# Optimization experiments

Hardware: AMD Instinct MI355X
Metric: run time of the kernel (lower is better)

Reference implementation:

```python
import jax, jax.numpy as jnp
import numpy as np

N_NODES = 50000
N_EDGES = 800000
D_FEAT = 128
UNITS = 128


def setup_inputs() -> dict:
    key = jax.random.key(0)
    k1, k2, k3, k4 = jax.random.split(key, 4)
    x = jax.random.normal(k1, (N_NODES, D_FEAT), dtype=jnp.float32)
    source = jax.random.randint(k2, (N_EDGES,), 0, N_NODES, dtype=jnp.int32)
    target = jax.random.randint(k3, (N_EDGES,), 0, N_NODES, dtype=jnp.int32)
    W = jax.random.normal(k4, (D_FEAT, UNITS), dtype=jnp.float32) * (1.0 / np.sqrt(D_FEAT))
    b = jnp.zeros((UNITS,), dtype=jnp.float32)
    return {"x": x, "source": source, "target": target, "W": W, "b": b}


def _degree(idx, n_nodes):
    # in/out degree = segment-sum of unit edge weights; clamp to >= 1 (no self loops)
    deg = jnp.zeros((n_nodes,), dtype=jnp.float32).at[idx].add(1.0)
    return jnp.maximum(deg, 1.0)


def reference(x, source, target, W, b):
    n = x.shape[0]
    # degree_normalization == "in_out": sender scale from out-degree, receiver from in-degree
    sender_scale = jax.lax.rsqrt(_degree(source, n))[:, None]      # [N, 1]
    receiver_scale = jax.lax.rsqrt(_degree(target, n))[:, None]    # [N, 1]
    normalized = sender_scale * x                                  # [N, D]
    source_bcast = normalized[source]                              # [E, D] gather
    pooled = jax.ops.segment_sum(source_bcast, target, num_segments=n)  # [N, D] scatter-add
    pooled = receiver_scale * pooled
    # Dense(units, activation='relu', use_bias=True)
    return jax.nn.relu(pooled @ W + b)
```

## Files before the change

kernel.cpp:

```cpp
#include <hip/hip_runtime.h>
#include <hip/hip_bf16.h>

#define N_FEAT 128
#define EPT 8
#define CHUNK 2048
#define BSHIFT 8
#define MAXRANGE 256
#define CAP 8192

typedef short bf16x8 __attribute__((ext_vector_type(8)));
typedef float f32x4  __attribute__((ext_vector_type(4)));

__device__ __forceinline__ unsigned short f2bf_rtne(float f) {
    unsigned u = __float_as_uint(f);
    u += 0x7fffu + ((u >> 16) & 1u);
    return (unsigned short)(u >> 16);
}
__device__ __forceinline__ float bf2f(unsigned short h) {
    return __uint_as_float((unsigned)h << 16);
}

__global__ __launch_bounds__(256) void scatter_kernel(const int* __restrict__ source,
                                                      const int* __restrict__ target,
                                                      int* __restrict__ curT,
                                                      int* __restrict__ curS,
                                                      unsigned int* __restrict__ pairsT,
                                                      unsigned char* __restrict__ srcB,
                                                      int E, int NB) {
    __shared__ unsigned int   lds_pairs[CHUNK];
    __shared__ unsigned short lds_sp[CHUNK];
    __shared__ int ct[MAXRANGE], cs[MAXRANGE];
    __shared__ int st[MAXRANGE], ss[MAXRANGE];
    __shared__ int gt[MAXRANGE], gs[MAXRANGE];
    int tid = threadIdx.x, b = blockIdx.x;
    int base = b * CHUNK;
    int cnt = E - base; if (cnt > CHUNK) cnt = CHUNK;

    ct[tid] = 0; cs[tid] = 0;
    __syncthreads();
    #pragma unroll
    for (int j = 0; j < EPT; ++j) {
        int e = base + j * 256 + tid;
        if (e < E) {
            atomicAdd(&ct[target[e] >> BSHIFT], 1);
            atomicAdd(&cs[source[e] >> BSHIFT], 1);
        }
    }
    __syncthreads();
    int vt = ct[tid], vs = cs[tid];
    st[tid] = vt; ss[tid] = vs;
    __syncthreads();
    #pragma unroll
    for (int off = 1; off < 256; off <<= 1) {
        int t1 = (tid >= off) ? st[tid - off] : 0;
        int t2 = (tid >= off) ? ss[tid - off] : 0;
        __syncthreads();
        st[tid] += t1; ss[tid] += t2;
        __syncthreads();
    }
    int et = st[tid] - vt, es = ss[tid] - vs;
    int gT = 0, gS = 0;
    if (tid < NB) {
        if (vt) gT = atomicAdd(&curT[tid], vt);
        if (vs) gS = atomicAdd(&curS[tid], vs);
    }
    __syncthreads();
    st[tid] = et; ss[tid] = es;
    ct[tid] = et; cs[tid] = es;
    gt[tid] = gT; gs[tid] = gS;
    __syncthreads();
    #pragma unroll
    for (int j = 0; j < EPT; ++j) {
        int e = base + j * 256 + tid;
        if (e < E) {
            int s = source[e], t = target[e];
            int k = t >> BSHIFT;
            int p = atomicAdd(&ct[k], 1);
            lds_pairs[p] = (unsigned)s | ((unsigned)t << 16);
            int k2 = s >> BSHIFT;
            int p2 = atomicAdd(&cs[k2], 1);
            lds_sp[p2] = (unsigned short)s;
        }
    }
    __syncthreads();
    for (int i = tid; i < cnt; i += 256) {
        unsigned w = lds_pairs[i];
        int k = w >> 24;
        pairsT[(size_t)k * CAP + gt[k] + (i - st[k])] = w;
        unsigned short sp = lds_sp[i];
        int k2 = sp >> 8;
        srcB[(size_t)k2 * CAP + gs[k2] + (i - ss[k2])] = (unsigned char)sp;
    }
}

__global__ __launch_bounds__(256) void prep_kernel(const unsigned char* __restrict__ srcB,
                                                   const unsigned int* __restrict__ pairsT,
                                                   const int* __restrict__ curT,
                                                   const int* __restrict__ curS,
                                                   const float* __restrict__ x,
                                                   const float* __restrict__ W,
                                                   unsigned short* __restrict__ xb,
                                                   int2* __restrict__ offs,
                                                   int* __restrict__ elist,
                                                   float* __restrict__ ri,
                                                   unsigned short* __restrict__ Whi,
                                                   unsigned short* __restrict__ Wlo,
                                                   int N, int NB) {
    __shared__ int hist[MAXRANGE];
    __shared__ int sb[MAXRANGE];
    __shared__ int excl[MAXRANGE];
    __shared__ int cur[MAXRANGE];
    __shared__ float so_l[MAXRANGE];
    int tid = threadIdx.x, b = blockIdx.x;

    if (b < NB) {
        hist[tid] = 0;
        __syncthreads();
        int cnt = curS[b];
        size_t base = (size_t)b * CAP;
        for (int i = tid; i < cnt; i += 256)
            atomicAdd(&hist[srcB[base + i]], 1);
        __syncthreads();
        {
            int d = hist[tid]; if (d < 1) d = 1;
            so_l[tid] = rsqrtf((float)d);
        }
        __syncthreads();
        int row0 = b << BSHIFT;
        int nrows = N - row0; if (nrows > 256) nrows = 256;
        if (nrows <= 0) return;
        int nf4 = nrows * (N_FEAT / 4);
        const float4* xr = (const float4*)(x + (size_t)row0 * N_FEAT);
        ushort4* xo = (ushort4*)(xb + (size_t)row0 * N_FEAT);
        for (int i = tid; i < nf4; i += 256) {
            float s = so_l[i >> 5];
            float4 v = xr[i];
            xo[i] = make_ushort4(f2bf_rtne(s * v.x), f2bf_rtne(s * v.y),
                                 f2bf_rtne(s * v.z), f2bf_rtne(s * v.w));
        }
    } else if (b < 2 * NB) {
        int bb = b - NB;
        hist[tid] = 0; cur[tid] = 0;
        __syncthreads();
        int cnt = curT[bb];
        int gbase = bb * CAP;
        for (int i = tid; i < cnt; i += 256)
            atomicAdd(&hist[(pairsT[(size_t)gbase + i] >> 16) & 255], 1);
        __syncthreads();
        int deg = hist[tid];
        sb[tid] = deg;
        __syncthreads();
        #pragma unroll
        for (int off = 1; off < 256; off <<= 1) {
            int t = (tid >= off) ? sb[tid - off] : 0;
            __syncthreads();
            sb[tid] += t;
            __syncthreads();
        }
        excl[tid] = sb[tid] - deg;
        __syncthreads();
        int node = (bb << BSHIFT) + tid;
        if (node < N) {
            int st0 = gbase + excl[tid];
            offs[node] = make_int2(st0, st0 + deg);
            int d = deg; if (d < 1) d = 1;
            ri[node] = rsqrtf((float)d);
        }
        for (int i = tid; i < cnt; i += 256) {
            unsigned w = pairsT[(size_t)gbase + i];
            int tl = (w >> 16) & 255;
            int pos = atomicAdd(&cur[tl], 1);
            elist[gbase + excl[tl] + pos] = (int)(w & 0xFFFFu);
        }
    } else {
        int idx = (b - 2 * NB) * 256 + tid;
        int lane = idx & 63;
        int ks = (idx >> 6) & 3;
        int ct2 = idx >> 8;
        int n  = ct2 * 16 + (lane & 15);
        int k0 = ks * 32 + (lane >> 4) * 8;
        unsigned short h[8], l[8];
        #pragma unroll
        for (int j = 0; j < 8; ++j) {
            float w = W[(k0 + j) * N_FEAT + n];
            unsigned short hh = f2bf_rtne(w);
            h[j] = hh;
            l[j] = f2bf_rtne(w - bf2f(hh));
        }
        size_t off = (size_t)idx * 8;
        *(ushort4*)(Whi + off)     = make_ushort4(h[0], h[1], h[2], h[3]);
        *(ushort4*)(Whi + off + 4) = make_ushort4(h[4], h[5], h[6], h[7]);
        *(ushort4*)(Wlo + off)     = make_ushort4(l[0], l[1], l[2], l[3]);
        *(ushort4*)(Wlo + off + 4) = make_ushort4(l[4], l[5], l[6], l[7]);
    }
}

__global__ void agg_kernel(const unsigned short* __restrict__ xb,
                           const int* __restrict__ elist,
                           const int2* __restrict__ offs,
                           const float* __restrict__ ri,
                           unsigned int* __restrict__ poolhi,
                           unsigned int* __restrict__ poollo,
                           int N) {
    int wave = (blockIdx.x * blockDim.x + threadIdx.x) >> 6;
    int lane = threadIdx.x & 63;
    if (wave >= N) return;
    int2 oe = offs[wave];
    int start = oe.x, end = oe.y;
    int col = lane * 2;

    float2 a0 = make_float2(0.f, 0.f), a1 = a0, a2 = a0, a3 = a0;
    int i = start;
    for (; i + 8 <= end; i += 8) {
        int e0 = __builtin_amdgcn_readfirstlane(elist[i]);
        int e1 = __builtin_amdgcn_readfirstlane(elist[i + 1]);
        int e2 = __builtin_amdgcn_readfirstlane(elist[i + 2]);
        int e3 = __builtin_amdgcn_readfirstlane(elist[i + 3]);
        int e4 = __builtin_amdgcn_readfirstlane(elist[i + 4]);
        int e5 = __builtin_amdgcn_readfirstlane(elist[i + 5]);
        int e6 = __builtin_amdgcn_readfirstlane(elist[i + 6]);
        int e7 = __builtin_amdgcn_readfirstlane(elist[i + 7]);
        unsigned u0 = *(const unsigned*)(xb + (size_t)e0 * N_FEAT + col);
        unsigned u1 = *(const unsigned*)(xb + (size_t)e1 * N_FEAT + col);
        unsigned u2 = *(const unsigned*)(xb + (size_t)e2 * N_FEAT + col);
        unsigned u3 = *(const unsigned*)(xb + (size_t)e3 * N_FEAT + col);
        unsigned u4 = *(const unsigned*)(xb + (size_t)e4 * N_FEAT + col);
        unsigned u5 = *(const unsigned*)(xb + (size_t)e5 * N_FEAT + col);
        unsigned u6 = *(const unsigned*)(xb + (size_t)e6 * N_FEAT + col);
        unsigned u7 = *(const unsigned*)(xb + (size_t)e7 * N_FEAT + col);
        a0.x += __uint_as_float(u0 << 16); a0.y += __uint_as_float(u0 & 0xffff0000u);
        a1.x += __uint_as_float(u1 << 16); a1.y += __uint_as_float(u1 & 0xffff0000u);
        a2.x += __uint_as_float(u2 << 16); a2.y += __uint_as_float(u2 & 0xffff0000u);
        a3.x += __uint_as_float(u3 << 16); a3.y += __uint_as_float(u3 & 0xffff0000u);
        a0.x += __uint_as_float(u4 << 16); a0.y += __uint_as_float(u4 & 0xffff0000u);
        a1.x += __uint_as_float(u5 << 16); a1.y += __uint_as_float(u5 & 0xffff0000u);
        a2.x += __uint_as_float(u6 << 16); a2.y += __uint_as_float(u6 & 0xffff0000u);
        a3.x += __uint_as_float(u7 << 16); a3.y += __uint_as_float(u7 & 0xffff0000u);
    }
    for (; i < end; ++i) {
        int e = __builtin_amdgcn_readfirstlane(elist[i]);
        unsigned u = *(const unsigned*)(xb + (size_t)e * N_FEAT + col);
        a0.x += __uint_as_float(u << 16); a0.y += __uint_as_float(u & 0xffff0000u);
    }
    float r = ri[wave];
    float vx = ((a0.x + a1.x) + (a2.x + a3.x)) * r;
    float vy = ((a0.y + a1.y) + (a2.y + a3.y)) * r;
    unsigned short hx = f2bf_rtne(vx), hy = f2bf_rtne(vy);
    unsigned short lx = f2bf_rtne(vx - bf2f(hx)), ly = f2bf_rtne(vy - bf2f(hy));
    size_t o = (size_t)wave * (N_FEAT / 2) + lane;
    poolhi[o] = (unsigned)hx | ((unsigned)hy << 16);
    poollo[o] = (unsigned)lx | ((unsigned)ly << 16);
}

__global__ __launch_bounds__(256) void gemm_mfma_kernel(const unsigned short* __restrict__ poolhi,
                                                        const unsigned short* __restrict__ poollo,
                                                        const unsigned short* __restrict__ Whi,
                                                        const unsigned short* __restrict__ Wlo,
                                                        const float* __restrict__ bias,
                                                        float* __restrict__ out,
                                                        int N) {
    int wave = threadIdx.x >> 6;
    int lane = threadIdx.x & 63;
    int quad = lane >> 4;
    int rowbase = blockIdx.x * 64 + wave * 16;
    int m = rowbase + (lane & 15);
    int mload = (m < N) ? m : 0;

    bf16x8 Ahi[4], Alo[4];
    const unsigned short* ah = poolhi + (size_t)mload * N_FEAT + quad * 8;
    const unsigned short* al = poollo + (size_t)mload * N_FEAT + quad * 8;
    #pragma unroll
    for (int ks = 0; ks < 4; ++ks) {
        Ahi[ks] = *(const bf16x8*)(ah + ks * 32);
        Alo[ks] = *(const bf16x8*)(al + ks * 32);
    }

    const bf16x8* BH = (const bf16x8*)Whi;
    const bf16x8* BL = (const bf16x8*)Wlo;

    #pragma unroll
    for (int ct = 0; ct < 8; ++ct) {
        f32x4 acc = {0.f, 0.f, 0.f, 0.f};
        #pragma unroll
        for (int ks = 0; ks < 4; ++ks) {
            bf16x8 bh = BH[(ct * 4 + ks) * 64 + lane];
            bf16x8 bl = BL[(ct * 4 + ks) * 64 + lane];
            acc = __builtin_amdgcn_mfma_f32_16x16x32_bf16(Ahi[ks], bh, acc, 0, 0, 0);
            acc = __builtin_amdgcn_mfma_f32_16x16x32_bf16(Alo[ks], bh, acc, 0, 0, 0);
            acc = __builtin_amdgcn_mfma_f32_16x16x32_bf16(Ahi[ks], bl, acc, 0, 0, 0);
        }
        int colc = ct * 16 + (lane & 15);
        float bv = bias[colc];
        #pragma unroll
        for (int reg = 0; reg < 4; ++reg) {
            int r = rowbase + quad * 4 + reg;
            if (r < N)
                out[(size_t)r * N_FEAT + colc] = fmaxf(acc[reg] + bv, 0.f);
        }
    }
}

extern "C" void kernel_launch(void* const* d_in, const int* in_sizes, int n_in,
                              void* d_out, int out_size, void* d_ws, size_t ws_size,
                              hipStream_t stream) {
    const float* x      = (const float*)d_in[0];
    const int*   source = (const int*)d_in[1];
    const int*   target = (const int*)d_in[2];
    const float* W      = (const float*)d_in[3];
    const float* bias   = (const float*)d_in[4];
    float*       out    = (float*)d_out;

    const int N = in_sizes[0] / N_FEAT;
    const int E = in_sizes[1];

    const int NB   = (N + MAXRANGE - 1) >> BSHIFT;
    const int NBLK = (E + CHUNK - 1) / CHUNK;

    uintptr_t p = (uintptr_t)d_ws;
    auto carve = [&](size_t bytes) {
        p = (p + 255) & ~(uintptr_t)255;
        uintptr_t r = p;
        p += bytes;
        return (void*)r;
    };
    int*            curs    = (int*)carve((size_t)2 * NB * sizeof(int));
    int*            curT    = curs;
    int*            curS    = curs + NB;
    unsigned int*   pairsT  = (unsigned int*)carve((size_t)NB * CAP * sizeof(unsigned int));
    int*            elist   = (int*)carve((size_t)NB * CAP * sizeof(int));
    unsigned char*  srcB    = (unsigned char*)carve((size_t)NB * CAP);
    float*          ri      = (float*)carve((size_t)N * sizeof(float));
    int2*           offs    = (int2*)carve((size_t)N * sizeof(int2));
    unsigned short* xb      = (unsigned short*)carve((size_t)N * N_FEAT * sizeof(unsigned short));
    unsigned int*   poolhi  = (unsigned int*)carve((size_t)N * (N_FEAT / 2) * sizeof(unsigned int));
    unsigned int*   poollo  = (unsigned int*)carve((size_t)N * (N_FEAT / 2) * sizeof(unsigned int));
    unsigned short* Whi     = (unsigned short*)carve((size_t)N_FEAT * N_FEAT * sizeof(unsigned short));
    unsigned short* Wlo     = (unsigned short*)carve((size_t)N_FEAT * N_FEAT * sizeof(unsigned short));
    (void)ws_size; (void)n_in; (void)out_size;

    (void)hipMemsetAsync(curs, 0, (size_t)2 * NB * sizeof(int), stream);

    scatter_kernel<<<NBLK, 256, 0, stream>>>(source, target, curT, curS, pairsT, srcB, E, NB);
    prep_kernel<<<2 * NB + 8, 256, 0, stream>>>(srcB, pairsT, curT, curS, x, W,
                                                xb, offs, elist, ri, Whi, Wlo, N, NB);
    agg_kernel<<<(N + 3) / 4, 256, 0, stream>>>(xb, elist, offs, ri, poolhi, poollo, N);
    gemm_mfma_kernel<<<(N + 63) / 64, 256, 0, stream>>>(
        (const unsigned short*)poolhi, (const unsigned short*)poollo,
        Whi, Wlo, bias, out, N);
}
```

Measured before the change: 174.9 us.

## Fuse neighbor aggregation into MFMA GEMM via shared-memory staging

Merges the aggregation and GEMM kernels into one. Each 256-thread block aggregates 16 nodes, four per wave, writes the hi/lo bf16 split of the pooled rows into padded LDS, then each wave computes two 16-column MFMA output tiles. This removes the global write and re-read of the pooled hi/lo buffers and one kernel launch. The scatter kernel also keeps source/target in registers instead of reloading them. In exchange, each block now has a barrier where waves wait on the slowest node's aggregation, and every block re-reads all of W.

```diff
diff --git a/kernel.cpp b/kernel.cpp
--- a/kernel.cpp
+++ b/kernel.cpp
@@ -7,6 +7,7 @@
 #define BSHIFT 8
 #define MAXRANGE 256
 #define CAP 8192
+#define LSTR 66
 
 typedef short bf16x8 __attribute__((ext_vector_type(8)));
 typedef float f32x4  __attribute__((ext_vector_type(4)));
@@ -36,14 +37,17 @@
     int base = b * CHUNK;
     int cnt = E - base; if (cnt > CHUNK) cnt = CHUNK;
 
+    int rs[EPT], rt[EPT];
     ct[tid] = 0; cs[tid] = 0;
     __syncthreads();
     #pragma unroll
     for (int j = 0; j < EPT; ++j) {
         int e = base + j * 256 + tid;
         if (e < E) {
-            atomicAdd(&ct[target[e] >> BSHIFT], 1);
-            atomicAdd(&cs[source[e] >> BSHIFT], 1);
+            int s = source[e], t = target[e];
+            rs[j] = s; rt[j] = t;
+            atomicAdd(&ct[t >> BSHIFT], 1);
+            atomicAdd(&cs[s >> BSHIFT], 1);
         }
     }
     __syncthreads();
@@ -73,7 +77,7 @@
     for (int j = 0; j < EPT; ++j) {
         int e = base + j * 256 + tid;
         if (e < E) {
-            int s = source[e], t = target[e];
+            int s = rs[j], t = rt[j];
             int k = t >> BSHIFT;
             int p = atomicAdd(&ct[k], 1);
             lds_pairs[p] = (unsigned)s | ((unsigned)t << 16);
@@ -195,91 +199,89 @@
     }
 }
 
-__global__ void agg_kernel(const unsigned short* __restrict__ xb,
-                           const int* __restrict__ elist,
-                           const int2* __restrict__ offs,
-                           const float* __restrict__ ri,
-                           unsigned int* __restrict__ poolhi,
-                           unsigned int* __restrict__ poollo,
-                           int N) {
-    int wave = (blockIdx.x * blockDim.x + threadIdx.x) >> 6;
-    int lane = threadIdx.x & 63;
-    if (wave >= N) return;
-    int2 oe = offs[wave];
-    int start = oe.x, end = oe.y;
-    int col = lane * 2;
-
-    float2 a0 = make_float2(0.f, 0.f), a1 = a0, a2 = a0, a3 = a0;
-    int i = start;
-    for (; i + 8 <= end; i += 8) {
-        int e0 = __builtin_amdgcn_readfirstlane(elist[i]);
-        int e1 = __builtin_amdgcn_readfirstlane(elist[i + 1]);
-        int e2 = __builtin_amdgcn_readfirstlane(elist[i + 2]);
-        int e3 = __builtin_amdgcn_readfirstlane(elist[i + 3]);
-        int e4 = __builtin_amdgcn_readfirstlane(elist[i + 4]);
-        int e5 = __builtin_amdgcn_readfirstlane(elist[i + 5]);
-        int e6 = __builtin_amdgcn_readfirstlane(elist[i + 6]);
-        int e7 = __builtin_amdgcn_readfirstlane(elist[i + 7]);
-        unsigned u0 = *(const unsigned*)(xb + (size_t)e0 * N_FEAT + col);
-        unsigned u1 = *(const unsigned*)(xb + (size_t)e1 * N_FEAT + col);
-        unsigned u2 = *(const unsigned*)(xb + (size_t)e2 * N_FEAT + col);
-        unsigned u3 = *(const unsigned*)(xb + (size_t)e3 * N_FEAT + col);
-        unsigned u4 = *(const unsigned*)(xb + (size_t)e4 * N_FEAT + col);
-        unsigned u5 = *(const unsigned*)(xb + (size_t)e5 * N_FEAT + col);
-        unsigned u6 = *(const unsigned*)(xb + (size_t)e6 * N_FEAT + col);
-        unsigned u7 = *(const unsigned*)(xb + (size_t)e7 * N_FEAT + col);
-        a0.x += __uint_as_float(u0 << 16); a0.y += __uint_as_float(u0 & 0xffff0000u);
-        a1.x += __uint_as_float(u1 << 16); a1.y += __uint_as_float(u1 & 0xffff0000u);
-        a2.x += __uint_as_float(u2 << 16); a2.y += __uint_as_float(u2 & 0xffff0000u);
-        a3.x += __uint_as_float(u3 << 16); a3.y += __uint_as_float(u3 & 0xffff0000u);
-        a0.x += __uint_as_float(u4 << 16); a0.y += __uint_as_float(u4 & 0xffff0000u);
-        a1.x += __uint_as_float(u5 << 16); a1.y += __uint_as_float(u5 & 0xffff0000u);
-        a2.x += __uint_as_float(u6 << 16); a2.y += __uint_as_float(u6 & 0xffff0000u);
-        a3.x += __uint_as_float(u7 << 16); a3.y += __uint_as_float(u7 & 0xffff0000u);
-    }
-    for (; i < end; ++i) {
-        int e = __builtin_amdgcn_readfirstlane(elist[i]);
-        unsigned u = *(const unsigned*)(xb + (size_t)e * N_FEAT + col);
-        a0.x += __uint_as_float(u << 16); a0.y += __uint_as_float(u & 0xffff0000u);
-    }
-    float r = ri[wave];
-    float vx = ((a0.x + a1.x) + (a2.x + a3.x)) * r;
-    float vy = ((a0.y + a1.y) + (a2.y + a3.y)) * r;
-    unsigned short hx = f2bf_rtne(vx), hy = f2bf_rtne(vy);
-    unsigned short lx = f2bf_rtne(vx - bf2f(hx)), ly = f2bf_rtne(vy - bf2f(hy));
-    size_t o = (size_t)wave * (N_FEAT / 2) + lane;
-    poolhi[o] = (unsigned)hx | ((unsigned)hy << 16);
-    poollo[o] = (unsigned)lx | ((unsigned)ly << 16);
-}
-
-__global__ __launch_bounds__(256) void gemm_mfma_kernel(const unsigned short* __restrict__ poolhi,
-                                                        const unsigned short* __restrict__ poollo,
-                                                        const unsigned short* __restrict__ Whi,
-                                                        const unsigned short* __restrict__ Wlo,
-                                                        const float* __restrict__ bias,
-                                                        float* __restrict__ out,
-                                                        int N) {
+__global__ __launch_bounds__(256) void agg_gemm_kernel(const unsigned short* __restrict__ xb,
+                                                       const int* __restrict__ elist,
+                                                       const int2* __restrict__ offs,
+                                                       const float* __restrict__ ri,
+                                                       const unsigned short* __restrict__ Whi,
+                                                       const unsigned short* __restrict__ Wlo,
+                                                       const float* __restrict__ bias,
+                                                       float* __restrict__ out,
+                                                       int N) {
+    __shared__ unsigned int hi_l[16 * LSTR];
+    __shared__ unsigned int lo_l[16 * LSTR];
     int wave = threadIdx.x >> 6;
     int lane = threadIdx.x & 63;
     int quad = lane >> 4;
-    int rowbase = blockIdx.x * 64 + wave * 16;
-    int m = rowbase + (lane & 15);
-    int mload = (m < N) ? m : 0;
+    int rowbase = blockIdx.x * 16;
+    int col = lane * 2;
+
+    #pragma unroll
+    for (int i = 0; i < 4; ++i) {
+        int r = wave * 4 + i;
+        int node = rowbase + r;
+        float vx = 0.f, vy = 0.f;
+        if (node < N) {
+            int2 oe = offs[node];
+            int start = oe.x, end = oe.y;
+            float2 a0 = make_float2(0.f, 0.f), a1 = a0, a2 = a0, a3 = a0;
+            int j = start;
+            for (; j + 8 <= end; j += 8) {
+                int e0 = __builtin_amdgcn_readfirstlane(elist[j]);
+                int e1 = __builtin_amdgcn_readfirstlane(elist[j + 1]);
+                int e2 = __builtin_amdgcn_readfirstlane(elist[j + 2]);
+                int e3 = __builtin_amdgcn_readfirstlane(elist[j + 3]);
+                int e4 = __builtin_amdgcn_readfirstlane(elist[j + 4]);
+                int e5 = __builtin_amdgcn_readfirstlane(elist[j + 5]);
+                int e6 = __builtin_amdgcn_readfirstlane(elist[j + 6]);
+                int e7 = __builtin_amdgcn_readfirstlane(elist[j + 7]);
+                unsigned u0 = *(const unsigned*)(xb + (size_t)e0 * N_FEAT + col);
+                unsigned u1 = *(const unsigned*)(xb + (size_t)e1 * N_FEAT + col);
+                unsigned u2 = *(const unsigned*)(xb + (size_t)e2 * N_FEAT + col);
+                unsigned u3 = *(const unsigned*)(xb + (size_t)e3 * N_FEAT + col);
+                unsigned u4 = *(const unsigned*)(xb + (size_t)e4 * N_FEAT + col);
+                unsigned u5 = *(const unsigned*)(xb + (size_t)e5 * N_FEAT + col);
+                unsigned u6 = *(const unsigned*)(xb + (size_t)e6 * N_FEAT + col);
+                unsigned u7 = *(const unsigned*)(xb + (size_t)e7 * N_FEAT + col);
+                a0.x += __uint_as_float(u0 << 16); a0.y += __uint_as_float(u0 & 0xffff0000u);
+                a1.x += __uint_as_float(u1 << 16); a1.y += __uint_as_float(u1 & 0xffff0000u);
+                a2.x += __uint_as_float(u2 << 16); a2.y += __uint_as_float(u2 & 0xffff0000u);
+                a3.x += __uint_as_float(u3 << 16); a3.y += __uint_as_float(u3 & 0xffff0000u);
+                a0.x += __uint_as_float(u4 << 16); a0.y += __uint_as_float(u4 & 0xffff0000u);
+                a1.x += __uint_as_float(u5 << 16); a1.y += __uint_as_float(u5 & 0xffff0000u);
+                a2.x += __uint_as_float(u6 << 16); a2.y += __uint_as_float(u6 & 0xffff0000u);
+                a3.x += __uint_as_float(u7 << 16); a3.y += __uint_as_float(u7 & 0xffff0000u);
+            }
+            for (; j < end; ++j) {
+                int e = __builtin_amdgcn_readfirstlane(elist[j]);
+                unsigned u = *(const unsigned*)(xb + (size_t)e * N_FEAT + col);
+                a0.x += __uint_as_float(u << 16); a0.y += __uint_as_float(u & 0xffff0000u);
+            }
+            float rr = ri[node];
+            vx = ((a0.x + a1.x) + (a2.x + a3.x)) * rr;
+            vy = ((a0.y + a1.y) + (a2.y + a3.y)) * rr;
+        }
+        unsigned short hx = f2bf_rtne(vx), hy = f2bf_rtne(vy);
+        unsigned short lx = f2bf_rtne(vx - bf2f(hx)), ly = f2bf_rtne(vy - bf2f(hy));
+        hi_l[r * LSTR + lane] = (unsigned)hx | ((unsigned)hy << 16);
+        lo_l[r * LSTR + lane] = (unsigned)lx | ((unsigned)ly << 16);
+    }
+    __syncthreads();
 
     bf16x8 Ahi[4], Alo[4];
-    const unsigned short* ah = poolhi + (size_t)mload * N_FEAT + quad * 8;
-    const unsigned short* al = poollo + (size_t)mload * N_FEAT + quad * 8;
+    int m = lane & 15;
     #pragma unroll
     for (int ks = 0; ks < 4; ++ks) {
-        Ahi[ks] = *(const bf16x8*)(ah + ks * 32);
-        Alo[ks] = *(const bf16x8*)(al + ks * 32);
-    }
-
+        int a = m * LSTR + ks * 16 + quad * 4;
+        Ahi[ks] = *(const bf16x8*)(hi_l + a);
+        Alo[ks] = *(const bf16x8*)(lo_l + a);
+    }
     const bf16x8* BH = (const bf16x8*)Whi;
     const bf16x8* BL = (const bf16x8*)Wlo;
 
     #pragma unroll
-    for (int ct = 0; ct < 8; ++ct) {
+    for (int c = 0; c < 2; ++c) {
+        int ct = wave * 2 + c;
         f32x4 acc = {0.f, 0.f, 0.f, 0.f};
         #pragma unroll
         for (int ks = 0; ks < 4; ++ks) {
@@ -289,7 +291,7 @@
             acc = __builtin_amdgcn_mfma_f32_16x16x32_bf16(Alo[ks], bh, acc, 0, 0, 0);
             acc = __builtin_amdgcn_mfma_f32_16x16x32_bf16(Ahi[ks], bl, acc, 0, 0, 0);
         }
-        int colc = ct * 16 + (lane & 15);
+        int colc = ct * 16 + m;
         float bv = bias[colc];
         #pragma unroll
         for (int reg = 0; reg < 4; ++reg) {
@@ -332,8 +334,6 @@
     float*          ri      = (float*)carve((size_t)N * sizeof(float));
     int2*           offs    = (int2*)carve((size_t)N * sizeof(int2));
     unsigned short* xb      = (unsigned short*)carve((size_t)N * N_FEAT * sizeof(unsigned short));
-    unsigned int*   poolhi  = (unsigned int*)carve((size_t)N * (N_FEAT / 2) * sizeof(unsigned int));
-    unsigned int*   poollo  = (unsigned int*)carve((size_t)N * (N_FEAT / 2) * sizeof(unsigned int));
     unsigned short* Whi     = (unsigned short*)carve((size_t)N_FEAT * N_FEAT * sizeof(unsigned short));
     unsigned short* Wlo     = (unsigned short*)carve((size_t)N_FEAT * N_FEAT * sizeof(unsigned short));
     (void)ws_size; (void)n_in; (void)out_size;
@@ -343,8 +343,6 @@
     scatter_kernel<<<NBLK, 256, 0, stream>>>(source, target, curT, curS, pairsT, srcB, E, NB);
     prep_kernel<<<2 * NB + 8, 256, 0, stream>>>(srcB, pairsT, curT, curS, x, W,
                                                 xb, offs, elist, ri, Whi, Wlo, N, NB);
-    agg_kernel<<<(N + 3) / 4, 256, 0, stream>>>(xb, elist, offs, ri, poolhi, poollo, N);
-    gemm_mfma_kernel<<<(N + 63) / 64, 256, 0, stream>>>(
-        (const unsigned short*)poolhi, (const unsigned short*)poollo,
-        Whi, Wlo, bias, out, N);
-}
+    agg_gemm_kernel<<<(N + 15) / 16, 256, 0, stream>>>(xb, elist, offs, ri,
+                                                       Whi, Wlo, bias, out, N);
+}
```

Measured after the change: 168.2 us. -3.8%, faster.
